# Kernel optimization log

Measured on AMD Instinct MI355X. Metric: run time of the kernel, lower is better.

Reference implementation:

```python
import jax, jax.numpy as jnp
import numpy as np

H = 256
N = 64           # d_state; diagonal SSM uses N//2 conjugate-pair modes
N2 = N // 2
B, L = 16, 4096
EPS = 1e-5


def layernorm(x, g, b):
    m = jnp.mean(x, axis=-1, keepdims=True)
    v = jnp.mean((x - m) ** 2, axis=-1, keepdims=True)
    return (x - m) / jnp.sqrt(v + EPS) * g + b


def s4_layer(u, log_dt, A_re, A_im, C_re, C_im, D, Wout, bout):
    # u: (B, L, H). Bidirectional diagonal S4 (S4D-style ZOH kernel), channels=1.
    Bb, Ll, Hh = u.shape
    dt = jnp.exp(log_dt)                       # (H,)
    A = A_re + 1j * A_im                       # (H, N2), Re(A) < 0
    dtA = dt[:, None] * A                      # (H, N2)
    # ZOH discretization folded into C:  C <- C * (exp(dtA) - 1) / A
    C = (C_re + 1j * C_im) * (jnp.exp(dtA) - 1.0) / A   # (2, H, N2)
    vand = jnp.exp(dtA[:, :, None] * jnp.arange(Ll))    # (H, N2, L)
    k = 2.0 * jnp.einsum('chn,hnl->chl', C, vand).real  # (2, H, L)
    k_fwd, k_bwd = k[0], k[1]
    # bidirectional: causal kernel + anticausal (flipped, shifted by L)
    z = jnp.zeros_like(k_fwd)
    k2 = jnp.concatenate([k_fwd, z], axis=-1) \
       + jnp.concatenate([z, k_bwd[:, ::-1]], axis=-1)  # (H, 2L)
    ut = jnp.transpose(u, (0, 2, 1))                    # (B, H, L)
    n_fft = 2 * Ll
    y = jnp.fft.irfft(jnp.fft.rfft(ut, n=n_fft) * jnp.fft.rfft(k2, n=n_fft), n=n_fft)[..., :Ll]
    y = y + ut * D[:, None]                             # skip connection
    y = jax.nn.gelu(y, approximate=False)
    y = jnp.transpose(y, (0, 2, 1))                     # (B, L, H)
    zz = y @ Wout + bout                                # (B, L, 2H)
    return zz[..., :Hh] * jax.nn.sigmoid(zz[..., Hh:])  # GLU output projection


def setup_inputs() -> dict:
    key = jax.random.key(0)
    ks = jax.random.split(key, 16)
    x = jax.random.normal(ks[0], (B, L, H), dtype=jnp.float32)
    log_dt = jnp.log(0.001) + jax.random.uniform(ks[1], (H,)) * (jnp.log(0.1) - jnp.log(0.001))
    A_re = -0.5 * jnp.ones((H, N2), dtype=jnp.float32)
    A_im = jnp.pi * jnp.broadcast_to(jnp.arange(N2, dtype=jnp.float32), (H, N2))
    C_re = jax.random.normal(ks[2], (2, H, N2), dtype=jnp.float32) * 0.5
    C_im = jax.random.normal(ks[3], (2, H, N2), dtype=jnp.float32) * 0.5
    Dskip = jax.random.normal(ks[4], (H,), dtype=jnp.float32)
    Wout = jax.random.normal(ks[5], (H, 2 * H), dtype=jnp.float32) / np.sqrt(H)
    bout = jnp.zeros((2 * H,), dtype=jnp.float32)
    ln1_g = jnp.ones((H,), jnp.float32); ln1_b = jnp.zeros((H,), jnp.float32)
    ln2_g = jnp.ones((H,), jnp.float32); ln2_b = jnp.zeros((H,), jnp.float32)
    W2 = jax.random.normal(ks[6], (H, 2 * H), dtype=jnp.float32) / np.sqrt(H)
    b2 = jnp.zeros((2 * H,), jnp.float32)
    W3 = jax.random.normal(ks[7], (2 * H, H), dtype=jnp.float32) / np.sqrt(2 * H)
    b3 = jnp.zeros((H,), jnp.float32)
    return dict(x=x, ln1_g=ln1_g, ln1_b=ln1_b, ln2_g=ln2_g, ln2_b=ln2_b,
                log_dt=log_dt, A_re=A_re, A_im=A_im, C_re=C_re, C_im=C_im,
                Dskip=Dskip, Wout=Wout, bout=bout, W2=W2, b2=b2, W3=W3, b3=b3)


def reference(x, ln1_g, ln1_b, ln2_g, ln2_b, log_dt, A_re, A_im, C_re, C_im,
              Dskip, Wout, bout, W2, b2, W3, b3):
    # residual S4 sub-block
    y = x
    h = layernorm(x, ln1_g, ln1_b)
    h = s4_layer(h, log_dt, A_re, A_im, C_re, C_im, Dskip, Wout, bout)
    x = y + h
    # residual MLP sub-block
    y = x
    h = layernorm(x, ln2_g, ln2_b)
    h = jax.nn.gelu(h @ W2 + b2, approximate=False)
    h = h @ W3 + b3
    return y + h
```

## Files before the change

### kernel.cpp

```cpp
#include <hip/hip_runtime.h>
#include <hip/hip_bf16.h>

typedef __attribute__((ext_vector_type(8))) short bf16x8;
typedef __attribute__((ext_vector_type(4))) float f32x4;

#define Hdim 256
#define NM 32
#define NB 16
#define LL 4096
#define PCH 256
#define NCH 16

#define OFF_Q    ((size_t)0)
#define OFF_KC   ((size_t)16777216)
#define OFF_WPM  ((size_t)50331648)
#define OFF_UT   ((size_t)67108864)
#define OFF_ZG   ((size_t)100663296)
#define OFF_M    ((size_t)67108864)
#define OFF_ZP   ((size_t)134217728)
#define OFF_G    ((size_t)150994944)
#define OFF_WTAB ((size_t)185073664)
#define OFF_WPT  ((size_t)185139200)
#define OFF_CE   ((size_t)185204736)
#define OFF_W1T  ((size_t)185335808)
#define OFF_W2T  ((size_t)185597952)
#define OFF_W3T  ((size_t)185860096)

typedef const __attribute__((address_space(1))) void* gas_p;
typedef __attribute__((address_space(3))) void* las_p;

__device__ __forceinline__ float gelu_f(float v) {
    float u = 0.7978845608028654f * fmaf(0.044715f * v * v, v, v);
    float uc = fminf(fmaxf(u, -15.f), 15.f);
    float e = __expf(2.f * uc);
    return 0.5f * v * (1.f + (e - 1.f) * __builtin_amdgcn_rcpf(e + 1.f));
}
__device__ __forceinline__ unsigned short f2bf(float f) {
    unsigned int u = __float_as_uint(f);
    u += 0x7fffu + ((u >> 16) & 1u);
    return (unsigned short)(u >> 16);
}
__device__ __forceinline__ float bf2f(unsigned short u) {
    return __uint_as_float((unsigned int)u << 16);
}

__device__ __forceinline__ bf16x8 fr(const unsigned short* lds, int row, int kcol) {
    return *(const bf16x8*)(lds + row * 64 + ((((kcol >> 3) ^ (row & 7)) << 3)));
}

template<int ROWS, int THREADS>
__device__ __forceinline__ void stage64(const unsigned short* __restrict__ src, int ld, int k0,
                                        unsigned short* lds, int t) {
    constexpr int EPI = THREADS * 8;
#pragma unroll
    for (int i = 0; i < (ROWS * 64) / EPI; i++) {
        int e = i * EPI + t * 8;
        int r = e >> 6;
        int k = (((e >> 3) & 7) ^ (r & 7)) << 3;
        const unsigned short* g = src + (size_t)r * ld + (k0 + k);
        unsigned short* l = lds + i * EPI + (t >> 6) * 512;
        __builtin_amdgcn_global_load_lds((gas_p)g, (las_p)l, 16, 0, 0);
    }
}

template<int ROWS, int THREADS>
__device__ __forceinline__ void stageUT(const unsigned short* __restrict__ UT, int h, int rbase,
                                        int k0, unsigned short* lds, int t) {
    constexpr int EPI = THREADS * 8;
#pragma unroll
    for (int i = 0; i < (ROWS * 64) / EPI; i++) {
        int e = i * EPI + t * 8;
        int r = e >> 6;
        int k = (((e >> 3) & 7) ^ (r & 7)) << 3;
        int row = rbase + r;
        const unsigned short* g = UT + ((size_t)((row >> 4) * Hdim + h)) * LL
                                  + (row & 15) * PCH + (k0 + k);
        unsigned short* l = lds + i * EPI + (t >> 6) * 512;
        __builtin_amdgcn_global_load_lds((gas_p)g, (las_p)l, 16, 0, 0);
    }
}

__global__ void k_tab(const float* __restrict__ logdt, const float* __restrict__ Are,
                      const float* __restrict__ Aim, const float* __restrict__ Cre,
                      const float* __restrict__ Cim, float2* __restrict__ wtab,
                      float2* __restrict__ wptab, float2* __restrict__ ceff) {
    int idx = blockIdx.x * blockDim.x + threadIdx.x;
    if (idx >= Hdim * NM) return;
    int h = idx >> 5;
    float dt = expf(logdt[h]);
    double dar = (double)dt * (double)Are[idx];
    double dai = (double)dt * (double)Aim[idx];
    double wm = exp(dar);
    double wr = wm * cos(dai), wi = wm * sin(dai);
    wtab[idx] = make_float2((float)wr, (float)wi);
    double pm = exp(dar * (double)PCH);
    double pai = dai * (double)PCH;
    wptab[idx] = make_float2((float)(pm * cos(pai)), (float)(pm * sin(pai)));
    double are = (double)Are[idx], aim = (double)Aim[idx];
    double den = are * are + aim * aim;
    double nr = wr - 1.0, ni = wi;
    double qr = (nr * are + ni * aim) / den;
    double qi = (ni * are - nr * aim) / den;
    for (int ch = 0; ch < 2; ch++) {
        double cr = (double)Cre[ch * Hdim * NM + idx];
        double ci = (double)Cim[ch * Hdim * NM + idx];
        ceff[ch * Hdim * NM + idx] = make_float2((float)(cr * qr - ci * qi),
                                                 (float)(cr * qi + ci * qr));
    }
}

__global__ void k_wt(const float* __restrict__ W1, const float* __restrict__ W2,
                     const float* __restrict__ W3, unsigned short* __restrict__ W1T,
                     unsigned short* __restrict__ W2T, unsigned short* __restrict__ W3T) {
    int t = blockIdx.x * 256 + threadIdx.x;
    int k = t >> 9, n = t & 511;
    W1T[n * 256 + k] = f2bf(W1[t]);
    W2T[n * 256 + k] = f2bf(W2[t]);
    int k3 = t >> 8, n3 = t & 255;
    W3T[n3 * 512 + k3] = f2bf(W3[t]);
}

__global__ __launch_bounds__(256) void k_abw(const float* __restrict__ logdt,
                                             const float* __restrict__ Are,
                                             const float* __restrict__ Aim,
                                             const float2* __restrict__ CE,
                                             unsigned short* __restrict__ Q,
                                             unsigned short* __restrict__ Wp,
                                             float* __restrict__ Kcat) {
    __shared__ float2 wpow[32][258];
    __shared__ float2 ce_s[64];
    int h = blockIdx.x;
    int part = blockIdx.y;
    int t = threadIdx.x;
    if (t < 64) ce_s[t] = CE[(t >> 5) * (Hdim * NM) + h * NM + (t & 31)];
    {
        int n = t >> 3, seg = t & 7;
        float dt = expf(logdt[h]);
        float dar = dt * Are[h * NM + n], dai = dt * Aim[h * NM + n];
        float em = expf(dar);
        float wr = em * cosf(dai), wi = em * sinf(dai);
        float ar = wr, ai = wi;
#pragma unroll
        for (int s = 0; s < 3; s++) { float nr = ar * ar - ai * ai, ni = 2.f * ar * ai; ar = nr; ai = ni; }
        float m = expf((float)seg * dar), ang = (float)seg * dai;
        float vr = m * cosf(ang), vi = m * sinf(ang);
        for (int q = 0; q < 32; q++) {
            wpow[n][seg + 8 * q] = make_float2(vr, vi);
            float nr2 = vr * ar - vi * ai;
            float ni2 = vr * ai + vi * ar;
            vr = nr2; vi = ni2;
        }
        if (seg == 0) wpow[n][256] = make_float2(vr, vi);
    }
    __syncthreads();
    if (part == 4) {
        float kfv = 0.f, kbv = 0.f;
#pragma unroll
        for (int n = 0; n < NM; n++) {
            float2 wv = wpow[n][t];
            float2 cf = ce_s[n], cb = ce_s[32 + n];
            kfv = fmaf(cf.x, wv.x, fmaf(-cf.y, wv.y, kfv));
            kbv = fmaf(cb.x, wv.x, fmaf(-cb.y, wv.y, kbv));
        }
        Kcat[(size_t)h * 512 + 255 + t] = 2.f * kfv;
        if (t < 255) Kcat[(size_t)h * 512 + 254 - t] = 2.f * kbv;
        if (t == 255) Kcat[(size_t)h * 512 + 511] = 0.f;
        return;
    }
    for (int jj = 0; jj < 32; jj++) {
        int j = part * 64 + jj * 2 + (t >> 7);
        int tq = t & 127;
        int n = (tq & 63) >> 1, reim = tq & 1;
        float2 c = (tq < 64) ? ce_s[n] : ce_s[32 + n];
        float2 wv = (tq < 64) ? wpow[n][j + 1] : wpow[n][255 - j];
        float re = c.x * wv.x - c.y * wv.y;
        float im = c.x * wv.y + c.y * wv.x;
        Q[((size_t)h * 256 + j) * 128 + tq] = f2bf(reim ? -2.f * im : 2.f * re);
    }
    for (int rr = 0; rr < 32; rr++) {
        int r = part * 32 + rr;
        int n = (r & 63) >> 1, reim = r & 1, dir = r >> 6;
        float2 wv = wpow[n][dir ? t : 255 - t];
        Wp[((size_t)h * 128 + r) * 256 + t] = f2bf(reim ? wv.y : wv.x);
    }
}

__global__ __launch_bounds__(256) void k_lntr(const float* __restrict__ x,
                                              const float* __restrict__ g,
                                              const float* __restrict__ bt,
                                              unsigned short* __restrict__ UT) {
    __shared__ unsigned short lds[256][65];
    int lt = blockIdx.x, b = blockIdx.y;
    int t = threadIdx.x;
    int lane = t & 63, w = t >> 6;
    float4 gg = ((const float4*)g)[lane];
    float4 bb = ((const float4*)bt)[lane];
#pragma unroll
    for (int q = 0; q < 16; q++) {
        int l = q * 4 + w;
        float4 v = ((const float4*)(x + ((size_t)(b * LL + lt * 64 + l)) * Hdim))[lane];
        float s = v.x + v.y + v.z + v.w;
        float ss = v.x * v.x + v.y * v.y + v.z * v.z + v.w * v.w;
#pragma unroll
        for (int o = 1; o < 64; o <<= 1) { s += __shfl_xor(s, o, 64); ss += __shfl_xor(ss, o, 64); }
        float mean = s * (1.0f / Hdim);
        float var = ss * (1.0f / Hdim) - mean * mean;
        float rstd = rsqrtf(var + 1e-5f);
        lds[lane * 4 + 0][l] = f2bf((v.x - mean) * rstd * gg.x + bb.x);
        lds[lane * 4 + 1][l] = f2bf((v.y - mean) * rstd * gg.y + bb.y);
        lds[lane * 4 + 2][l] = f2bf((v.z - mean) * rstd * gg.z + bb.z);
        lds[lane * 4 + 3][l] = f2bf((v.w - mean) * rstd * gg.w + bb.w);
    }
    __syncthreads();
    for (int q = 0; q < 64; q++) {
        int idx = q * 256 + t;
        int hh = idx >> 6, ll = idx & 63;
        UT[((size_t)(b * Hdim + hh)) * LL + lt * 64 + ll] = lds[hh][ll];
    }
}

__global__ void k_ln_bf(const unsigned short* __restrict__ x, const float* __restrict__ g,
                        const float* __restrict__ bt, unsigned short* __restrict__ out) {
    int row = blockIdx.x * 4 + (threadIdx.x >> 6);
    int lane = threadIdx.x & 63;
    ushort4 u4 = ((const ushort4*)(x + (size_t)row * Hdim))[lane];
    float vx = bf2f(u4.x), vy = bf2f(u4.y), vz = bf2f(u4.z), vw = bf2f(u4.w);
    float s = vx + vy + vz + vw;
    float ss = vx * vx + vy * vy + vz * vz + vw * vw;
#pragma unroll
    for (int o = 1; o < 64; o <<= 1) { s += __shfl_xor(s, o, 64); ss += __shfl_xor(ss, o, 64); }
    float mean = s * (1.0f / Hdim);
    float var = ss * (1.0f / Hdim) - mean * mean;
    float rstd = rsqrtf(var + 1e-5f);
    float4 gg = ((const float4*)g)[lane];
    float4 bb = ((const float4*)bt)[lane];
    ushort4 o;
    o.x = f2bf((vx - mean) * rstd * gg.x + bb.x);
    o.y = f2bf((vy - mean) * rstd * gg.y + bb.y);
    o.z = f2bf((vz - mean) * rstd * gg.z + bb.z);
    o.w = f2bf((vw - mean) * rstd * gg.w + bb.w);
    ((ushort4*)(out + (size_t)row * Hdim))[lane] = o;
}

__global__ __launch_bounds__(512) void k_zgemm(const unsigned short* __restrict__ UT,
                                               const unsigned short* __restrict__ Wp,
                                               unsigned short* __restrict__ Zg) {
    __shared__ unsigned short As[256 * 64];
    __shared__ unsigned short Bs[128 * 64];
    int h = blockIdx.x;
    int t = threadIdx.x;
    int w = t >> 6, lane = t & 63;
    int m0 = (w & 3) * 64;
    int nb = (w >> 2) * 64;
    int lr = lane & 15, lk = (lane >> 4) * 8;
    f32x4 acc[4][4];
#pragma unroll
    for (int i = 0; i < 4; i++)
#pragma unroll
        for (int jx = 0; jx < 4; jx++) acc[i][jx] = (f32x4){0.f, 0.f, 0.f, 0.f};
    for (int k0 = 0; k0 < 256; k0 += 64) {
        stageUT<256, 512>(UT, h, 0, k0, As, t);
        stage64<128, 512>(Wp + (size_t)h * 128 * 256, 256, k0, Bs, t);
        __syncthreads();
#pragma unroll
        for (int kk = 0; kk < 64; kk += 32) {
            bf16x8 a[4], b[4];
#pragma unroll
            for (int mi = 0; mi < 4; mi++) a[mi] = fr(As, m0 + mi * 16 + lr, kk + lk);
#pragma unroll
            for (int nf = 0; nf < 4; nf++) b[nf] = fr(Bs, nb + nf * 16 + lr, kk + lk);
#pragma unroll
            for (int mi = 0; mi < 4; mi++)
#pragma unroll
                for (int nf = 0; nf < 4; nf++)
                    acc[mi][nf] = __builtin_amdgcn_mfma_f32_16x16x32_bf16(a[mi], b[nf], acc[mi][nf], 0, 0, 0);
        }
        __syncthreads();
    }
#pragma unroll
    for (int mi = 0; mi < 4; mi++)
#pragma unroll
        for (int nf = 0; nf < 4; nf++) {
            int col = nb + nf * 16 + lr;
#pragma unroll
            for (int r = 0; r < 4; r++) {
                int row = m0 + mi * 16 + (lane >> 4) * 4 + r;
                Zg[((size_t)h * 256 + row) * 128 + col] = f2bf(acc[mi][nf][r]);
            }
        }
}

__global__ void k_prefix2(const unsigned short* __restrict__ Zg, const float2* __restrict__ wptab,
                          unsigned short* __restrict__ ZP) {
    int t = blockIdx.x * 256 + threadIdx.x;
    int n = t & 31;
    int h = (t >> 5) & 255;
    int b = (t >> 13) & 15;
    int dir = (t >> 17) & 1;
    float2 wp = wptab[h * NM + n];
    float sr = 0.f, si = 0.f;
    int ro = dir ? 64 + 2 * n : 2 * n;
    if (dir == 0) {
        for (int c = 0; c < NCH; c++) {
            size_t base = ((size_t)h * 256 + b * NCH + c) * 128;
            ZP[base + ro] = f2bf(sr);
            ZP[base + ro + 1] = f2bf(si);
            float zr = bf2f(Zg[base + ro]), zi = bf2f(Zg[base + ro + 1]);
            float nr = fmaf(wp.x, sr, fmaf(-wp.y, si, zr));
            float ni = fmaf(wp.y, sr, fmaf(wp.x, si, zi));
            sr = nr; si = ni;
        }
    } else {
        for (int c = NCH - 1; c >= 0; c--) {
            size_t base = ((size_t)h * 256 + b * NCH + c) * 128;
            ZP[base + ro] = f2bf(sr);
            ZP[base + ro + 1] = f2bf(si);
            float zr = bf2f(Zg[base + ro]), zi = bf2f(Zg[base + ro + 1]);
            float nr = fmaf(wp.x, sr, fmaf(-wp.y, si, zr));
            float ni = fmaf(wp.y, sr, fmaf(wp.x, si, zi));
            sr = nr; si = ni;
        }
    }
}

__global__ __launch_bounds__(512) void k_conv(const unsigned short* __restrict__ UT,
                                              const unsigned short* __restrict__ ZP,
                                              const unsigned short* __restrict__ Q,
                                              const float* __restrict__ Kcat,
                                              const float* __restrict__ Dsk,
                                              unsigned short* __restrict__ Yt) {
    __shared__ unsigned short As[128 * 64];
    __shared__ unsigned short Bs[256 * 64];
    __shared__ float kcs[512];
    int wgid = ((int)blockIdx.x % 8) * 64 + (int)blockIdx.x / 8;
    int h = wgid >> 1;
    int mbase = (wgid & 1) * 128;
    int t = threadIdx.x;
    int w = t >> 6, lane = t & 63;
    int m0 = (w & 1) * 64;
    int nb = (w >> 1) * 64;
    int lr = lane & 15, lk = (lane >> 4) * 8;
    float dsk = Dsk[h];
    kcs[t] = Kcat[(size_t)h * 512 + t];
    __syncthreads();
    f32x4 acc[4][4];
#pragma unroll
    for (int i = 0; i < 4; i++)
#pragma unroll
        for (int jx = 0; jx < 4; jx++) acc[i][jx] = (f32x4){0.f, 0.f, 0.f, 0.f};
    for (int k0 = 0; k0 < 256; k0 += 64) {
        stageUT<128, 512>(UT, h, mbase, k0, As, t);
#pragma unroll
        for (int gq = 0; gq < 4; gq++) {
            int e = gq * 4096 + t * 8;
            int j = e >> 6;
            int i0 = k0 + (e & 63);
            union { bf16x8 v; unsigned short u[8]; } pk;
#pragma unroll
            for (int q = 0; q < 8; q++) {
                int i = i0 + q;
                float f = kcs[255 + j - i];
                if (i == j) f += dsk;
                pk.u[q] = f2bf(f);
            }
            *(bf16x8*)(Bs + j * 64 + (((((e & 63) >> 3)) ^ (j & 7)) << 3)) = pk.v;
        }
        __syncthreads();
#pragma unroll
        for (int kk = 0; kk < 64; kk += 32) {
            bf16x8 a[4], b[4];
#pragma unroll
            for (int mi = 0; mi < 4; mi++) a[mi] = fr(As, m0 + mi * 16 + lr, kk + lk);
#pragma unroll
            for (int nf = 0; nf < 4; nf++) b[nf] = fr(Bs, nb + nf * 16 + lr, kk + lk);
#pragma unroll
            for (int mi = 0; mi < 4; mi++)
#pragma unroll
                for (int nf = 0; nf < 4; nf++)
                    acc[mi][nf] = __builtin_amdgcn_mfma_f32_16x16x32_bf16(a[mi], b[nf], acc[mi][nf], 0, 0, 0);
        }
        __syncthreads();
    }
    for (int k0 = 0; k0 < 128; k0 += 64) {
        stage64<128, 512>(ZP + ((size_t)h * 256 + mbase) * 128, 128, k0, As, t);
        stage64<256, 512>(Q + (size_t)h * 256 * 128, 128, k0, Bs, t);
        __syncthreads();
#pragma unroll
        for (int kk = 0; kk < 64; kk += 32) {
            bf16x8 a[4], b[4];
#pragma unroll
            for (int mi = 0; mi < 4; mi++) a[mi] = fr(As, m0 + mi * 16 + lr, kk + lk);
#pragma unroll
            for (int nf = 0; nf < 4; nf++) b[nf] = fr(Bs, nb + nf * 16 + lr, kk + lk);
#pragma unroll
            for (int mi = 0; mi < 4; mi++)
#pragma unroll
                for (int nf = 0; nf < 4; nf++)
                    acc[mi][nf] = __builtin_amdgcn_mfma_f32_16x16x32_bf16(a[mi], b[nf], acc[mi][nf], 0, 0, 0);
        }
        __syncthreads();
    }
#pragma unroll
    for (int mi = 0; mi < 4; mi++)
#pragma unroll
        for (int nf = 0; nf < 4; nf++) {
            int col = nb + nf * 16 + lr;
#pragma unroll
            for (int r = 0; r < 4; r++) {
                int row = mbase + m0 + mi * 16 + (lane >> 4) * 4 + r;
                Yt[(size_t)h * 65536 + row * 256 + col] = f2bf(gelu_f(acc[mi][nf][r]));
            }
        }
}

__global__ void k_trg(const unsigned short* __restrict__ Yt, unsigned short* __restrict__ G) {
    __shared__ unsigned short lds[64][65];
    int bc = blockIdx.x;
    int h0 = blockIdx.y * 64, j0 = blockIdx.z * 64;
    int t = threadIdx.x;
#pragma unroll
    for (int q = 0; q < 16; q++) {
        int idx = q * 256 + t;
        int hh = idx >> 6, jj = idx & 63;
        lds[hh][jj] = Yt[(size_t)(h0 + hh) * 65536 + bc * 256 + j0 + jj];
    }
    __syncthreads();
    int b = bc >> 4, c = bc & 15;
#pragma unroll
    for (int q = 0; q < 16; q++) {
        int idx = q * 256 + t;
        int jj = idx >> 6, hh = idx & 63;
        G[((size_t)(b * LL + c * PCH + j0 + jj)) * Hdim + h0 + hh] = lds[hh][jj];
    }
}

__global__ __launch_bounds__(1024) void k_gemm1(const unsigned short* __restrict__ Gm,
                                                const unsigned short* __restrict__ W1T,
                                                const float* __restrict__ bo,
                                                const float* __restrict__ xin,
                                                unsigned short* __restrict__ X2) {
    __shared__ unsigned short As[128 * 64];
    __shared__ unsigned short BsA[256 * 64];
    __shared__ unsigned short BsB[256 * 64];
    int t = threadIdx.x;
    int w = t >> 6, lane = t & 63;
    int m0w = (w & 1) * 64;
    int n0w = (w >> 1) * 32;
    int lr = lane & 15, lk = (lane >> 4) * 8;
    int mblk = blockIdx.x * 128;
    const unsigned short* Ab  = Gm + (size_t)mblk * 256;
    f32x4 acc[4][4];
#pragma unroll
    for (int i = 0; i < 4; i++)
#pragma unroll
        for (int j = 0; j < 4; j++) acc[i][j] = (f32x4){0.f, 0.f, 0.f, 0.f};
    for (int k0 = 0; k0 < 256; k0 += 64) {
        stage64<128, 1024>(Ab, 256, k0, As, t);
        stage64<256, 1024>(W1T, 256, k0, BsA, t);
        stage64<256, 1024>(W1T + (size_t)256 * 256, 256, k0, BsB, t);
        __syncthreads();
#pragma unroll
        for (int kk = 0; kk < 64; kk += 32) {
            bf16x8 a[4], bA[2], bB[2];
#pragma unroll
            for (int mi = 0; mi < 4; mi++)
                a[mi] = fr(As, m0w + mi * 16 + lr, kk + lk);
#pragma unroll
            for (int nf = 0; nf < 2; nf++) {
                bA[nf] = fr(BsA, n0w + nf * 16 + lr, kk + lk);
                bB[nf] = fr(BsB, n0w + nf * 16 + lr, kk + lk);
            }
#pragma unroll
            for (int mi = 0; mi < 4; mi++)
#pragma unroll
                for (int nf = 0; nf < 2; nf++) {
                    acc[mi][nf] = __builtin_amdgcn_mfma_f32_16x16x32_bf16(a[mi], bA[nf], acc[mi][nf], 0, 0, 0);
                    acc[mi][nf + 2] = __builtin_amdgcn_mfma_f32_16x16x32_bf16(a[mi], bB[nf], acc[mi][nf + 2], 0, 0, 0);
                }
        }
        __syncthreads();
    }
#pragma unroll
    for (int mi = 0; mi < 4; mi++)
#pragma unroll
        for (int nf = 0; nf < 2; nf++) {
            int col = n0w + nf * 16 + lr;
            float biasA = bo[col], biasB = bo[col + 256];
#pragma unroll
            for (int r = 0; r < 4; r++) {
                int row = mblk + m0w + mi * 16 + (lane >> 4) * 4 + r;
                float zzA = acc[mi][nf][r] + biasA;
                float zzB = acc[mi][nf + 2][r] + biasB;
                float v = zzA * __builtin_amdgcn_rcpf(1.0f + __expf(-zzB));
                size_t idx = (size_t)row * 256 + col;
                X2[idx] = f2bf(xin[idx] + v);
            }
        }
}

__global__ __launch_bounds__(1024) void k_gemm2(const unsigned short* __restrict__ T2,
                                                const unsigned short* __restrict__ W2T,
                                                const float* __restrict__ b2,
                                                unsigned short* __restrict__ Mo) {
    __shared__ unsigned short As[128 * 64];
    __shared__ unsigned short Bs[512 * 64];
    int t = threadIdx.x;
    int w = t >> 6, lane = t & 63;
    int m0w = (w & 1) * 64;
    int n0w = (w >> 1) * 64;
    int lr = lane & 15, lk = (lane >> 4) * 8;
    int mblk = blockIdx.x * 128;
    const unsigned short* Ab = T2 + (size_t)mblk * 256;
    f32x4 acc[4][4];
#pragma unroll
    for (int i = 0; i < 4; i++)
#pragma unroll
        for (int j = 0; j < 4; j++) acc[i][j] = (f32x4){0.f, 0.f, 0.f, 0.f};
    for (int k0 = 0; k0 < 256; k0 += 64) {
        stage64<128, 1024>(Ab, 256, k0, As, t);
        stage64<512, 1024>(W2T, 256, k0, Bs, t);
        __syncthreads();
#pragma unroll
        for (int kk = 0; kk < 64; kk += 32) {
            bf16x8 a[4], b[4];
#pragma unroll
            for (int mi = 0; mi < 4; mi++)
                a[mi] = fr(As, m0w + mi * 16 + lr, kk + lk);
#pragma unroll
            for (int nf = 0; nf < 4; nf++)
                b[nf] = fr(Bs, n0w + nf * 16 + lr, kk + lk);
#pragma unroll
            for (int mi = 0; mi < 4; mi++)
#pragma unroll
                for (int nf = 0; nf < 4; nf++)
                    acc[mi][nf] = __builtin_amdgcn_mfma_f32_16x16x32_bf16(a[mi], b[nf], acc[mi][nf], 0, 0, 0);
        }
        __syncthreads();
    }
#pragma unroll
    for (int mi = 0; mi < 4; mi++)
#pragma unroll
        for (int nf = 0; nf < 4; nf++) {
            int col = n0w + nf * 16 + lr;
            float bias = b2[col];
#pragma unroll
            for (int r = 0; r < 4; r++) {
                int row = mblk + m0w + mi * 16 + (lane >> 4) * 4 + r;
                Mo[(size_t)row * 512 + col] = f2bf(gelu_f(acc[mi][nf][r] + bias));
            }
        }
}

__global__ __launch_bounds__(1024) void k_gemm3(const unsigned short* __restrict__ Mb,
                                                const unsigned short* __restrict__ W3T,
                                                const float* __restrict__ b3,
                                                const unsigned short* __restrict__ X2,
                                                float* __restrict__ out) {
    __shared__ unsigned short As[128 * 64];
    __shared__ unsigned short Bs[256 * 64];
    int t = threadIdx.x;
    int w = t >> 6, lane = t & 63;
    int m0w = (w & 1) * 64;
    int n0w = (w >> 1) * 32;
    int lr = lane & 15, lk = (lane >> 4) * 8;
    int mblk = blockIdx.x * 128;
    const unsigned short* Ab = Mb + (size_t)mblk * 512;
    f32x4 acc[4][2];
#pragma unroll
    for (int i = 0; i < 4; i++) { acc[i][0] = (f32x4){0.f,0.f,0.f,0.f}; acc[i][1] = (f32x4){0.f,0.f,0.f,0.f}; }
    for (int k0 = 0; k0 < 512; k0 += 64) {
        stage64<128, 1024>(Ab, 512, k0, As, t);
        stage64<256, 1024>(W3T, 512, k0, Bs, t);
        __syncthreads();
#pragma unroll
        for (int kk = 0; kk < 64; kk += 32) {
            bf16x8 a[4], b[2];
#pragma unroll
            for (int mi = 0; mi < 4; mi++)
                a[mi] = fr(As, m0w + mi * 16 + lr, kk + lk);
#pragma unroll
            for (int nf = 0; nf < 2; nf++)
                b[nf] = fr(Bs, n0w + nf * 16 + lr, kk + lk);
#pragma unroll
            for (int mi = 0; mi < 4; mi++)
#pragma unroll
                for (int nf = 0; nf < 2; nf++)
                    acc[mi][nf] = __builtin_amdgcn_mfma_f32_16x16x32_bf16(a[mi], b[nf], acc[mi][nf], 0, 0, 0);
        }
        __syncthreads();
    }
#pragma unroll
    for (int mi = 0; mi < 4; mi++)
#pragma unroll
        for (int nf = 0; nf < 2; nf++) {
            int col = n0w + nf * 16 + lr;
            float bias = b3[col];
#pragma unroll
            for (int r = 0; r < 4; r++) {
                int row = mblk + m0w + mi * 16 + (lane >> 4) * 4 + r;
                size_t idx = (size_t)row * 256 + col;
                out[idx] = bf2f(X2[idx]) + acc[mi][nf][r] + bias;
            }
        }
}

extern "C" void kernel_launch(void* const* d_in, const int* in_sizes, int n_in,
                              void* d_out, int out_size, void* d_ws, size_t ws_size,
                              hipStream_t stream) {
    const float* x     = (const float*)d_in[0];
    const float* ln1g  = (const float*)d_in[1];
    const float* ln1b  = (const float*)d_in[2];
    const float* ln2g  = (const float*)d_in[3];
    const float* ln2b  = (const float*)d_in[4];
    const float* logdt = (const float*)d_in[5];
    const float* Are   = (const float*)d_in[6];
    const float* Aim   = (const float*)d_in[7];
    const float* Cre   = (const float*)d_in[8];
    const float* Cim   = (const float*)d_in[9];
    const float* Dsk   = (const float*)d_in[10];
    const float* Wout  = (const float*)d_in[11];
    const float* bo    = (const float*)d_in[12];
    const float* W2    = (const float*)d_in[13];
    const float* b2    = (const float*)d_in[14];
    const float* W3    = (const float*)d_in[15];
    const float* b3    = (const float*)d_in[16];

    char* ws = (char*)d_ws;
    unsigned short* Q    = (unsigned short*)(ws + OFF_Q);
    float*          Kc   = (float*)(ws + OFF_KC);
    unsigned short* Wp   = (unsigned short*)(ws + OFF_WPM);
    unsigned short* X2   = (unsigned short*)(ws + OFF_Q);
    unsigned short* UT   = (unsigned short*)(ws + OFF_UT);
    unsigned short* Zg   = (unsigned short*)(ws + OFF_ZG);
    unsigned short* Yt   = (unsigned short*)(ws + OFF_ZG);
    unsigned short* Mb   = (unsigned short*)(ws + OFF_M);
    unsigned short* ZP   = (unsigned short*)(ws + OFF_ZP);
    unsigned short* G    = (unsigned short*)(ws + OFF_G);
    float2*         WT   = (float2*)(ws + OFF_WTAB);
    float2*         WPT  = (float2*)(ws + OFF_WPT);
    float2*         CE   = (float2*)(ws + OFF_CE);
    unsigned short* W1T  = (unsigned short*)(ws + OFF_W1T);
    unsigned short* W2T  = (unsigned short*)(ws + OFF_W2T);
    unsigned short* W3T  = (unsigned short*)(ws + OFF_W3T);

    k_tab<<<32, 256, 0, stream>>>(logdt, Are, Aim, Cre, Cim, WT, WPT, CE);
    k_wt<<<512, 256, 0, stream>>>(Wout, W2, W3, W1T, W2T, W3T);
    k_lntr<<<dim3(64, 16), 256, 0, stream>>>(x, ln1g, ln1b, UT);
    k_abw<<<dim3(256, 5), 256, 0, stream>>>(logdt, Are, Aim, CE, Q, Wp, Kc);
    k_zgemm<<<256, 512, 0, stream>>>(UT, Wp, Zg);
    k_prefix2<<<1024, 256, 0, stream>>>(Zg, WPT, ZP);
    k_conv<<<512, 512, 0, stream>>>(UT, ZP, Q, Kc, Dsk, Yt);
    k_trg<<<dim3(256, 4, 4), 256, 0, stream>>>(Yt, G);
    k_gemm1<<<512, 1024, 0, stream>>>(G, W1T, bo, x, X2);
    k_ln_bf<<<NB * LL / 4, 256, 0, stream>>>(X2, ln2g, ln2b, G);
    k_gemm2<<<512, 1024, 0, stream>>>(G, W2T, b2, Mb);
    k_gemm3<<<512, 1024, 0, stream>>>(Mb, W3T, b3, X2, (float*)d_out);
}
```

Baseline: 234.7 us.

## Fuse second LayerNorm into GLU GEMM epilogue and split MLP GEMM over N

The separate LayerNorm kernel is removed. Its work moves into the gemm1 epilogue: each 128-row block already holds all 256 output columns, so row sums and sums of squares are reduced with shuffles and LDS, and the normalized bf16 activations are written in place over the G buffer. The write is safe because each block reads only its own rows of G, and only before it overwrites them. This removes one launch and a full read/write pass of the activation tensor, at the cost of extra LDS syncs and register use in gemm1. Separately, gemm2 is split into two N-halves of 256 columns with 512-thread blocks, which doubles the grid and halves the B tile in LDS.

Result: slower. 248.0 us (+5.7%).

```diff
diff --git a/kernel.cpp b/kernel.cpp
--- a/kernel.cpp
+++ b/kernel.cpp
@@ -219,29 +219,6 @@
     }
 }
 
-__global__ void k_ln_bf(const unsigned short* __restrict__ x, const float* __restrict__ g,
-                        const float* __restrict__ bt, unsigned short* __restrict__ out) {
-    int row = blockIdx.x * 4 + (threadIdx.x >> 6);
-    int lane = threadIdx.x & 63;
-    ushort4 u4 = ((const ushort4*)(x + (size_t)row * Hdim))[lane];
-    float vx = bf2f(u4.x), vy = bf2f(u4.y), vz = bf2f(u4.z), vw = bf2f(u4.w);
-    float s = vx + vy + vz + vw;
-    float ss = vx * vx + vy * vy + vz * vz + vw * vw;
-#pragma unroll
-    for (int o = 1; o < 64; o <<= 1) { s += __shfl_xor(s, o, 64); ss += __shfl_xor(ss, o, 64); }
-    float mean = s * (1.0f / Hdim);
-    float var = ss * (1.0f / Hdim) - mean * mean;
-    float rstd = rsqrtf(var + 1e-5f);
-    float4 gg = ((const float4*)g)[lane];
-    float4 bb = ((const float4*)bt)[lane];
-    ushort4 o;
-    o.x = f2bf((vx - mean) * rstd * gg.x + bb.x);
-    o.y = f2bf((vy - mean) * rstd * gg.y + bb.y);
-    o.z = f2bf((vz - mean) * rstd * gg.z + bb.z);
-    o.w = f2bf((vw - mean) * rstd * gg.w + bb.w);
-    ((ushort4*)(out + (size_t)row * Hdim))[lane] = o;
-}
-
 __global__ __launch_bounds__(512) void k_zgemm(const unsigned short* __restrict__ UT,
                                                const unsigned short* __restrict__ Wp,
                                                unsigned short* __restrict__ Zg) {
@@ -434,11 +411,14 @@
     }
 }
 
-__global__ __launch_bounds__(1024) void k_gemm1(const unsigned short* __restrict__ Gm,
+__global__ __launch_bounds__(1024) void k_gemm1(const unsigned short* Gm,
                                                 const unsigned short* __restrict__ W1T,
                                                 const float* __restrict__ bo,
                                                 const float* __restrict__ xin,
-                                                unsigned short* __restrict__ X2) {
+                                                const float* __restrict__ ln2g,
+                                                const float* __restrict__ ln2b,
+                                                unsigned short* __restrict__ X2,
+                                                unsigned short* T2out) {
     __shared__ unsigned short As[128 * 64];
     __shared__ unsigned short BsA[256 * 64];
     __shared__ unsigned short BsB[256 * 64];
@@ -447,8 +427,9 @@
     int m0w = (w & 1) * 64;
     int n0w = (w >> 1) * 32;
     int lr = lane & 15, lk = (lane >> 4) * 8;
+    int q4 = lane >> 4;
     int mblk = blockIdx.x * 128;
-    const unsigned short* Ab  = Gm + (size_t)mblk * 256;
+    const unsigned short* Ab = Gm + (size_t)mblk * 256;
     f32x4 acc[4][4];
 #pragma unroll
     for (int i = 0; i < 4; i++)
@@ -480,6 +461,12 @@
         }
         __syncthreads();
     }
+    unsigned short xb[4][2][4];
+    float psum[4][4], psq[4][4];
+#pragma unroll
+    for (int mi = 0; mi < 4; mi++)
+#pragma unroll
+        for (int r = 0; r < 4; r++) { psum[mi][r] = 0.f; psq[mi][r] = 0.f; }
 #pragma unroll
     for (int mi = 0; mi < 4; mi++)
 #pragma unroll
@@ -488,37 +475,91 @@
             float biasA = bo[col], biasB = bo[col + 256];
 #pragma unroll
             for (int r = 0; r < 4; r++) {
-                int row = mblk + m0w + mi * 16 + (lane >> 4) * 4 + r;
+                int row = mblk + m0w + mi * 16 + q4 * 4 + r;
                 float zzA = acc[mi][nf][r] + biasA;
                 float zzB = acc[mi][nf + 2][r] + biasB;
                 float v = zzA * __builtin_amdgcn_rcpf(1.0f + __expf(-zzB));
                 size_t idx = (size_t)row * 256 + col;
-                X2[idx] = f2bf(xin[idx] + v);
-            }
-        }
-}
-
-__global__ __launch_bounds__(1024) void k_gemm2(const unsigned short* __restrict__ T2,
-                                                const unsigned short* __restrict__ W2T,
-                                                const float* __restrict__ b2,
-                                                unsigned short* __restrict__ Mo) {
+                unsigned short us = f2bf(xin[idx] + v);
+                X2[idx] = us;
+                xb[mi][nf][r] = us;
+                float xf = bf2f(us);
+                psum[mi][r] += xf;
+                psq[mi][r] = fmaf(xf, xf, psq[mi][r]);
+            }
+        }
+#pragma unroll
+    for (int mi = 0; mi < 4; mi++)
+#pragma unroll
+        for (int r = 0; r < 4; r++) {
+            float s = psum[mi][r], q = psq[mi][r];
+#pragma unroll
+            for (int o = 1; o < 16; o <<= 1) { s += __shfl_xor(s, o, 64); q += __shfl_xor(q, o, 64); }
+            psum[mi][r] = s; psq[mi][r] = q;
+        }
+    float* red  = (float*)As;
+    float* redq = red + 1024;
+    float* mr   = redq + 1024;
+    __syncthreads();
+    if (lr == 0) {
+#pragma unroll
+        for (int mi = 0; mi < 4; mi++)
+#pragma unroll
+            for (int r = 0; r < 4; r++) {
+                int rl = m0w + mi * 16 + q4 * 4 + r;
+                red[rl * 8 + (w >> 1)]  = psum[mi][r];
+                redq[rl * 8 + (w >> 1)] = psq[mi][r];
+            }
+    }
+    __syncthreads();
+    if (t < 128) {
+        float s = 0.f, q = 0.f;
+#pragma unroll
+        for (int j = 0; j < 8; j++) { s += red[t * 8 + j]; q += redq[t * 8 + j]; }
+        float mean = s * (1.0f / 256.0f);
+        float var = q * (1.0f / 256.0f) - mean * mean;
+        mr[t * 2] = mean;
+        mr[t * 2 + 1] = rsqrtf(var + 1e-5f);
+    }
+    __syncthreads();
+#pragma unroll
+    for (int mi = 0; mi < 4; mi++)
+#pragma unroll
+        for (int nf = 0; nf < 2; nf++) {
+            int col = n0w + nf * 16 + lr;
+            float g2 = ln2g[col], b2v = ln2b[col];
+#pragma unroll
+            for (int r = 0; r < 4; r++) {
+                int rl = m0w + mi * 16 + q4 * 4 + r;
+                float mean = mr[rl * 2], rstd = mr[rl * 2 + 1];
+                float xf = bf2f(xb[mi][nf][r]);
+                T2out[(size_t)(mblk + rl) * 256 + col] = f2bf((xf - mean) * rstd * g2 + b2v);
+            }
+        }
+}
+
+__global__ __launch_bounds__(512) void k_gemm2(const unsigned short* __restrict__ T2,
+                                               const unsigned short* __restrict__ W2T,
+                                               const float* __restrict__ b2,
+                                               unsigned short* __restrict__ Mo) {
     __shared__ unsigned short As[128 * 64];
-    __shared__ unsigned short Bs[512 * 64];
+    __shared__ unsigned short Bs[256 * 64];
     int t = threadIdx.x;
     int w = t >> 6, lane = t & 63;
     int m0w = (w & 1) * 64;
     int n0w = (w >> 1) * 64;
     int lr = lane & 15, lk = (lane >> 4) * 8;
-    int mblk = blockIdx.x * 128;
+    int mblk = blockIdx.x * 128, nblk = blockIdx.y * 256;
     const unsigned short* Ab = T2 + (size_t)mblk * 256;
+    const unsigned short* Bb = W2T + (size_t)nblk * 256;
     f32x4 acc[4][4];
 #pragma unroll
     for (int i = 0; i < 4; i++)
 #pragma unroll
         for (int j = 0; j < 4; j++) acc[i][j] = (f32x4){0.f, 0.f, 0.f, 0.f};
     for (int k0 = 0; k0 < 256; k0 += 64) {
-        stage64<128, 1024>(Ab, 256, k0, As, t);
-        stage64<512, 1024>(W2T, 256, k0, Bs, t);
+        stage64<128, 512>(Ab, 256, k0, As, t);
+        stage64<256, 512>(Bb, 256, k0, Bs, t);
         __syncthreads();
 #pragma unroll
         for (int kk = 0; kk < 64; kk += 32) {
@@ -541,7 +582,7 @@
     for (int mi = 0; mi < 4; mi++)
 #pragma unroll
         for (int nf = 0; nf < 4; nf++) {
-            int col = n0w + nf * 16 + lr;
+            int col = nblk + n0w + nf * 16 + lr;
             float bias = b2[col];
 #pragma unroll
             for (int r = 0; r < 4; r++) {
@@ -651,8 +692,7 @@
     k_prefix2<<<1024, 256, 0, stream>>>(Zg, WPT, ZP);
     k_conv<<<512, 512, 0, stream>>>(UT, ZP, Q, Kc, Dsk, Yt);
     k_trg<<<dim3(256, 4, 4), 256, 0, stream>>>(Yt, G);
-    k_gemm1<<<512, 1024, 0, stream>>>(G, W1T, bo, x, X2);
-    k_ln_bf<<<NB * LL / 4, 256, 0, stream>>>(X2, ln2g, ln2b, G);
-    k_gemm2<<<512, 1024, 0, stream>>>(G, W2T, b2, Mb);
+    k_gemm1<<<512, 1024, 0, stream>>>(G, W1T, bo, x, ln2g, ln2b, X2, G);
+    k_gemm2<<<dim3(512, 2), 512, 0, stream>>>(G, W2T, b2, Mb);
     k_gemm3<<<512, 1024, 0, stream>>>(Mb, W3T, b3, X2, (float*)d_out);
 }
```

## Fuse MLP up- and down-projection GEMMs keeping hidden activations in LDS

Applied to the files above, without the earlier changes.

Merges the W2 GEMM+GELU kernel and the W3 GEMM kernel into one kernel. Each 128-row block computes the 512-wide hidden activation in two 256-column chunks, writes them as bf16 into a swizzled shared-memory buffer, and immediately consumes them in the W3 GEMM. This removes the global write and reread of the 64 MB-scale hidden tensor and one launch. In exchange the block uses more LDS (96 KB), which can limit occupancy, and the A tile is restaged once per chunk.

Result: slower. 288.1 us (+22.8%).

```diff
diff --git a/kernel.cpp b/kernel.cpp
--- a/kernel.cpp
+++ b/kernel.cpp
@@ -16,7 +16,6 @@
 #define OFF_WPM  ((size_t)50331648)
 #define OFF_UT   ((size_t)67108864)
 #define OFF_ZG   ((size_t)100663296)
-#define OFF_M    ((size_t)67108864)
 #define OFF_ZP   ((size_t)134217728)
 #define OFF_G    ((size_t)150994944)
 #define OFF_WTAB ((size_t)185073664)
@@ -498,96 +497,85 @@
         }
 }
 
-__global__ __launch_bounds__(1024) void k_gemm2(const unsigned short* __restrict__ T2,
-                                                const unsigned short* __restrict__ W2T,
-                                                const float* __restrict__ b2,
-                                                unsigned short* __restrict__ Mo) {
-    __shared__ unsigned short As[128 * 64];
-    __shared__ unsigned short Bs[512 * 64];
-    int t = threadIdx.x;
-    int w = t >> 6, lane = t & 63;
-    int m0w = (w & 1) * 64;
-    int n0w = (w >> 1) * 64;
-    int lr = lane & 15, lk = (lane >> 4) * 8;
-    int mblk = blockIdx.x * 128;
-    const unsigned short* Ab = T2 + (size_t)mblk * 256;
-    f32x4 acc[4][4];
-#pragma unroll
-    for (int i = 0; i < 4; i++)
-#pragma unroll
-        for (int j = 0; j < 4; j++) acc[i][j] = (f32x4){0.f, 0.f, 0.f, 0.f};
-    for (int k0 = 0; k0 < 256; k0 += 64) {
-        stage64<128, 1024>(Ab, 256, k0, As, t);
-        stage64<512, 1024>(W2T, 256, k0, Bs, t);
-        __syncthreads();
-#pragma unroll
-        for (int kk = 0; kk < 64; kk += 32) {
-            bf16x8 a[4], b[4];
-#pragma unroll
-            for (int mi = 0; mi < 4; mi++)
-                a[mi] = fr(As, m0w + mi * 16 + lr, kk + lk);
-#pragma unroll
-            for (int nf = 0; nf < 4; nf++)
-                b[nf] = fr(Bs, n0w + nf * 16 + lr, kk + lk);
-#pragma unroll
-            for (int mi = 0; mi < 4; mi++)
-#pragma unroll
-                for (int nf = 0; nf < 4; nf++)
-                    acc[mi][nf] = __builtin_amdgcn_mfma_f32_16x16x32_bf16(a[mi], b[nf], acc[mi][nf], 0, 0, 0);
-        }
-        __syncthreads();
-    }
-#pragma unroll
-    for (int mi = 0; mi < 4; mi++)
-#pragma unroll
-        for (int nf = 0; nf < 4; nf++) {
-            int col = n0w + nf * 16 + lr;
-            float bias = b2[col];
-#pragma unroll
-            for (int r = 0; r < 4; r++) {
-                int row = mblk + m0w + mi * 16 + (lane >> 4) * 4 + r;
-                Mo[(size_t)row * 512 + col] = f2bf(gelu_f(acc[mi][nf][r] + bias));
-            }
-        }
-}
-
-__global__ __launch_bounds__(1024) void k_gemm3(const unsigned short* __restrict__ Mb,
-                                                const unsigned short* __restrict__ W3T,
-                                                const float* __restrict__ b3,
-                                                const unsigned short* __restrict__ X2,
-                                                float* __restrict__ out) {
-    __shared__ unsigned short As[128 * 64];
-    __shared__ unsigned short Bs[256 * 64];
+__global__ __launch_bounds__(1024) void k_mlp(const unsigned short* __restrict__ T2,
+                                              const unsigned short* __restrict__ W2T,
+                                              const float* __restrict__ b2,
+                                              const unsigned short* __restrict__ W3T,
+                                              const float* __restrict__ b3,
+                                              const unsigned short* __restrict__ X2,
+                                              float* __restrict__ out) {
+    __shared__ unsigned short Ml[4 * 128 * 64];
+    __shared__ unsigned short Bs3[256 * 64];
+    unsigned short* As  = Ml;
+    unsigned short* Bs2 = Ml + 8192;
     int t = threadIdx.x;
     int w = t >> 6, lane = t & 63;
     int m0w = (w & 1) * 64;
     int n0w = (w >> 1) * 32;
     int lr = lane & 15, lk = (lane >> 4) * 8;
+    int q4 = lane >> 4;
     int mblk = blockIdx.x * 128;
-    const unsigned short* Ab = Mb + (size_t)mblk * 512;
-    f32x4 acc[4][2];
-#pragma unroll
-    for (int i = 0; i < 4; i++) { acc[i][0] = (f32x4){0.f,0.f,0.f,0.f}; acc[i][1] = (f32x4){0.f,0.f,0.f,0.f}; }
-    for (int k0 = 0; k0 < 512; k0 += 64) {
-        stage64<128, 1024>(Ab, 512, k0, As, t);
-        stage64<256, 1024>(W3T, 512, k0, Bs, t);
-        __syncthreads();
-#pragma unroll
-        for (int kk = 0; kk < 64; kk += 32) {
-            bf16x8 a[4], b[2];
-#pragma unroll
-            for (int mi = 0; mi < 4; mi++)
-                a[mi] = fr(As, m0w + mi * 16 + lr, kk + lk);
-#pragma unroll
-            for (int nf = 0; nf < 2; nf++)
-                b[nf] = fr(Bs, n0w + nf * 16 + lr, kk + lk);
-#pragma unroll
-            for (int mi = 0; mi < 4; mi++)
-#pragma unroll
-                for (int nf = 0; nf < 2; nf++)
-                    acc[mi][nf] = __builtin_amdgcn_mfma_f32_16x16x32_bf16(a[mi], b[nf], acc[mi][nf], 0, 0, 0);
-        }
-        __syncthreads();
+    const unsigned short* Ab = T2 + (size_t)mblk * 256;
+    f32x4 acc3[4][2];
+#pragma unroll
+    for (int i = 0; i < 4; i++) { acc3[i][0] = (f32x4){0.f,0.f,0.f,0.f}; acc3[i][1] = (f32x4){0.f,0.f,0.f,0.f}; }
+    for (int ch = 0; ch < 2; ch++) {
+        f32x4 acc2[4][2];
+#pragma unroll
+        for (int i = 0; i < 4; i++) { acc2[i][0] = (f32x4){0.f,0.f,0.f,0.f}; acc2[i][1] = (f32x4){0.f,0.f,0.f,0.f}; }
+        for (int k0 = 0; k0 < 256; k0 += 64) {
+            stage64<128, 1024>(Ab, 256, k0, As, t);
+            stage64<256, 1024>(W2T + (size_t)(ch * 256) * 256, 256, k0, Bs2, t);
+            __syncthreads();
+#pragma unroll
+            for (int kk = 0; kk < 64; kk += 32) {
+                bf16x8 a[4], b[2];
+#pragma unroll
+                for (int mi = 0; mi < 4; mi++) a[mi] = fr(As, m0w + mi * 16 + lr, kk + lk);
+#pragma unroll
+                for (int nf = 0; nf < 2; nf++) b[nf] = fr(Bs2, n0w + nf * 16 + lr, kk + lk);
+#pragma unroll
+                for (int mi = 0; mi < 4; mi++)
+#pragma unroll
+                    for (int nf = 0; nf < 2; nf++)
+                        acc2[mi][nf] = __builtin_amdgcn_mfma_f32_16x16x32_bf16(a[mi], b[nf], acc2[mi][nf], 0, 0, 0);
+            }
+            __syncthreads();
+        }
+#pragma unroll
+        for (int mi = 0; mi < 4; mi++)
+#pragma unroll
+            for (int nf = 0; nf < 2; nf++) {
+                int col = n0w + nf * 16 + lr;
+                float bias = b2[ch * 256 + col];
+#pragma unroll
+                for (int r = 0; r < 4; r++) {
+                    int row = m0w + mi * 16 + q4 * 4 + r;
+                    int c = col & 63;
+                    Ml[(col >> 6) * 8192 + row * 64 + ((((c >> 3) ^ (row & 7)) << 3)) + (c & 7)]
+                        = f2bf(gelu_f(acc2[mi][nf][r] + bias));
+                }
+            }
+        __syncthreads();
+        for (int k0 = 0; k0 < 256; k0 += 64) {
+            stage64<256, 1024>(W3T, 512, ch * 256 + k0, Bs3, t);
+            __syncthreads();
+#pragma unroll
+            for (int kk = 0; kk < 64; kk += 32) {
+                bf16x8 a[4], b[2];
+#pragma unroll
+                for (int mi = 0; mi < 4; mi++)
+                    a[mi] = fr(Ml + (k0 >> 6) * 8192, m0w + mi * 16 + lr, kk + lk);
+#pragma unroll
+                for (int nf = 0; nf < 2; nf++) b[nf] = fr(Bs3, n0w + nf * 16 + lr, kk + lk);
+#pragma unroll
+                for (int mi = 0; mi < 4; mi++)
+#pragma unroll
+                    for (int nf = 0; nf < 2; nf++)
+                        acc3[mi][nf] = __builtin_amdgcn_mfma_f32_16x16x32_bf16(a[mi], b[nf], acc3[mi][nf], 0, 0, 0);
+            }
+            __syncthreads();
+        }
     }
 #pragma unroll
     for (int mi = 0; mi < 4; mi++)
@@ -597,9 +585,9 @@
             float bias = b3[col];
 #pragma unroll
             for (int r = 0; r < 4; r++) {
-                int row = mblk + m0w + mi * 16 + (lane >> 4) * 4 + r;
+                int row = mblk + m0w + mi * 16 + q4 * 4 + r;
                 size_t idx = (size_t)row * 256 + col;
-                out[idx] = bf2f(X2[idx]) + acc[mi][nf][r] + bias;
+                out[idx] = bf2f(X2[idx]) + acc3[mi][nf][r] + bias;
             }
         }
 }
@@ -633,7 +621,6 @@
     unsigned short* UT   = (unsigned short*)(ws + OFF_UT);
     unsigned short* Zg   = (unsigned short*)(ws + OFF_ZG);
     unsigned short* Yt   = (unsigned short*)(ws + OFF_ZG);
-    unsigned short* Mb   = (unsigned short*)(ws + OFF_M);
     unsigned short* ZP   = (unsigned short*)(ws + OFF_ZP);
     unsigned short* G    = (unsigned short*)(ws + OFF_G);
     float2*         WT   = (float2*)(ws + OFF_WTAB);
@@ -653,6 +640,5 @@
     k_trg<<<dim3(256, 4, 4), 256, 0, stream>>>(Yt, G);
     k_gemm1<<<512, 1024, 0, stream>>>(G, W1T, bo, x, X2);
     k_ln_bf<<<NB * LL / 4, 256, 0, stream>>>(X2, ln2g, ln2b, G);
-    k_gemm2<<<512, 1024, 0, stream>>>(G, W2T, b2, Mb);
-    k_gemm3<<<512, 1024, 0, stream>>>(Mb, W3T, b3, X2, (float*)d_out);
-}
+    k_mlp<<<512, 1024, 0, stream>>>(G, W2T, b2, W3T, b3, X2, (float*)d_out);
+}
```
